# Optimization experiments

Hardware: AMD Instinct MI355X
Metric: run time of the kernel (lower is better)

## Reference

```python
import jax, jax.numpy as jnp
import numpy as np

D_MODEL = 128
D_STATE = 16
KCONV = 3
SQUEEZE = 16
NEIGH = 27
D_INNER = 2 * D_MODEL            # 256
C_CONV = D_INNER // SQUEEZE      # 16 conv3d output channels
D_SEQ = C_CONV * NEIGH           # 432 selective-scan channel dim
DT_RANK = int(np.ceil((D_MODEL // SQUEEZE * NEIGH) / 16))  # 14
LN_EPS = 1e-5


def setup_inputs() -> dict:
    key = jax.random.key(0)
    ks = jax.random.split(key, 10)
    B, Dd, H, W = 2, 16, 16, 16
    x = jax.random.normal(ks[0], (B, Dd, H, W, D_MODEL), dtype=jnp.float32)
    w_in = jax.random.normal(ks[1], (2 * D_INNER, D_MODEL), dtype=jnp.float32) * 0.02
    conv_w = jax.random.normal(ks[2], (C_CONV, SQUEEZE, KCONV, KCONV, KCONV), dtype=jnp.float32) * 0.05
    conv_b = jnp.zeros((C_CONV,), dtype=jnp.float32)
    x_proj_w = jax.random.normal(ks[3], (DT_RANK + 2 * D_STATE, D_SEQ), dtype=jnp.float32) * 0.05
    s = DT_RANK ** -0.5
    dt_w = jax.random.uniform(ks[4], (D_SEQ, DT_RANK), minval=-s, maxval=s, dtype=jnp.float32)
    # dt bias = inverse-softplus of dt ~ LogUniform[1e-3, 0.1]
    dt = jnp.exp(jax.random.uniform(ks[5], (D_SEQ,), dtype=jnp.float32)
                 * (np.log(0.1) - np.log(1e-3)) + np.log(1e-3))
    dt_b = dt + jnp.log(-jnp.expm1(-dt))
    A_logs = jnp.broadcast_to(jnp.log(jnp.arange(1, D_STATE + 1, dtype=jnp.float32)),
                              (D_SEQ, D_STATE)).copy()
    Ds = jnp.ones((D_SEQ,), dtype=jnp.float32)
    w_fold = jax.random.normal(ks[6], (D_INNER, D_SEQ), dtype=jnp.float32) * 0.05
    ln_g = jnp.ones((D_INNER,), dtype=jnp.float32)
    ln_b = jnp.zeros((D_INNER,), dtype=jnp.float32)
    w_out = jax.random.normal(ks[7], (D_MODEL, D_INNER), dtype=jnp.float32) * 0.05
    return dict(x=x, w_in=w_in, conv_w=conv_w, conv_b=conv_b, x_proj_w=x_proj_w,
                dt_w=dt_w, dt_b=dt_b, A_logs=A_logs, Ds=Ds, w_fold=w_fold,
                ln_g=ln_g, ln_b=ln_b, w_out=w_out)


def _selective_scan(u, delta, A, Bm, Cm, Dskip, delta_bias):
    # u, delta: (B, Dch, L); A: (Dch, N); Bm, Cm: (B, N, L); Dskip: (Dch,)
    delta = jax.nn.softplus(delta + delta_bias[None, :, None])
    a = jnp.exp(delta[..., None] * A[None, :, None, :])                     # (B,Dch,L,N)
    b = (delta * u)[..., None] * jnp.swapaxes(Bm, 1, 2)[:, None, :, :]      # (B,Dch,L,N)

    def combine(c1, c2):
        a1, b1 = c1
        a2, b2 = c2
        return a1 * a2, a2 * b1 + b2

    _, h = jax.lax.associative_scan(combine, (a, b), axis=2)                # (B,Dch,L,N)
    y = jnp.einsum('bdln,bnl->bdl', h, Cm)
    return y + Dskip[None, :, None] * u


def _unfold3(x):
    # x: (B, C, D, H, W) -> (B, C*27, D, H, W), channel-major, offset-minor
    B, C, Dd, H, W = x.shape
    p = KCONV // 2
    xp = jnp.pad(x, ((0, 0), (0, 0), (p, p), (p, p), (p, p)))
    taps = jnp.stack([xp[:, :, i:i + Dd, j:j + H, k:k + W]
                      for i in range(KCONV) for j in range(KCONV) for k in range(KCONV)],
                     axis=2)  # (B, C, 27, D, H, W)
    return taps.reshape(B, C * NEIGH, Dd, H, W)


def _forward(x, w_in, conv_w, conv_b, x_proj_w, dt_w, dt_b, A_logs, Ds,
             w_fold, ln_g, ln_b, w_out):
    B, Dd, H, W, _ = x.shape
    L = Dd * H * W
    xz = x @ w_in.T                                   # (B,D,H,W,512)
    xp, z = jnp.split(xz, 2, axis=-1)
    xc = jnp.transpose(xp, (0, 4, 1, 2, 3))           # (B,256,D,H,W)
    xc = jax.lax.conv_general_dilated(
        xc, conv_w, window_strides=(1, 1, 1), padding='SAME',
        dimension_numbers=('NCDHW', 'OIDHW', 'NCDHW'),
        feature_group_count=C_CONV) + conv_b[None, :, None, None, None]
    xc = jax.nn.silu(xc)                              # (B,16,D,H,W)
    xu = _unfold3(xc)                                 # (B,432,D,H,W)
    xs = xu.reshape(B, D_SEQ, L)
    x_dbl = jnp.einsum('bdl,cd->bcl', xs, x_proj_w)   # (B,46,L)
    dts = x_dbl[:, :DT_RANK]
    Bm = x_dbl[:, DT_RANK:DT_RANK + D_STATE]
    Cm = x_dbl[:, DT_RANK + D_STATE:]
    dts = jnp.einsum('brl,dr->bdl', dts, dt_w)        # (B,432,L)
    A = -jnp.exp(A_logs)
    y = _selective_scan(xs, dts, A, Bm, Cm, Ds, dt_b)  # (B,432,L)
    y = jnp.swapaxes(y, 1, 2).reshape(B, Dd, H, W, D_SEQ)
    y = y @ w_fold.T                                   # (B,D,H,W,256)
    mu = jnp.mean(y, axis=-1, keepdims=True)
    var = jnp.var(y, axis=-1, keepdims=True)
    y = (y - mu) * jax.lax.rsqrt(var + LN_EPS) * ln_g + ln_b
    y = y * jax.nn.silu(z)
    return y @ w_out.T                                 # (B,D,H,W,128)


def reference(x, w_in, conv_w, conv_b, x_proj_w, dt_w, dt_b, A_logs, Ds,
              w_fold, ln_g, ln_b, w_out):
    return _forward(x, w_in, conv_w, conv_b, x_proj_w, dt_w, dt_b, A_logs, Ds,
                    w_fold, ln_g, ln_b, w_out)
```

## Files before the change

kernel.cpp:

```cpp
#include <hip/hip_runtime.h>
#include <hip/hip_bf16.h>

#define DM     128
#define DSTATE 16
#define DINNER 256
#define CCONV  16
#define NEIGH  27
#define DSEQ   432
#define DTRANK 14
#define LVOL   4096
#define BATCH  2
#define NTOK   8192

typedef __attribute__((ext_vector_type(8))) unsigned short ushort8_t;
typedef __attribute__((ext_vector_type(8))) short short8_t;
typedef __attribute__((ext_vector_type(4))) float f32x4_t;

__device__ __forceinline__ float bf2f(unsigned short u) {
    union { unsigned int i; float f; } v; v.i = ((unsigned int)u) << 16; return v.f;
}
__device__ __forceinline__ unsigned short f2b(float f) {
    __hip_bfloat16 hb = __float2bfloat16(f);
    return *(unsigned short*)&hb;
}

__global__ void k_wprep(const float* __restrict__ w_in, const float* __restrict__ w_fold,
                        const float* __restrict__ w_out, float2* __restrict__ wint2,
                        unsigned short* __restrict__ wfb, unsigned short* __restrict__ wob) {
    int idx = blockIdx.x * 256 + threadIdx.x;
    if (idx < 32768) {
        int j = idx >> 8, t = idx & 255;
        wint2[idx] = make_float2(w_in[t * 128 + j], w_in[(t + 256) * 128 + j]);
    } else if (idx < 32768 + 114688) {
        int local = idx - 32768;
        int o = local / 448, dk = local - o * 448;
        wfb[local] = (dk < 432) ? f2b(w_fold[o * 432 + dk]) : (unsigned short)0;
    } else if (idx < 32768 + 114688 + 32768) {
        int local = idx - 32768 - 114688;
        wob[local] = f2b(w_out[local]);
    }
}

__global__ void k_inproj(const float* __restrict__ x, const float2* __restrict__ wint2,
                         float* __restrict__ xpt, float* __restrict__ zbuf) {
    int t = threadIdx.x;
    int tokbase = blockIdx.x * 16;
    int b = tokbase >> 12, lb = tokbase & 4095;
    __shared__ float xs_[16][128];
    for (int idx = t; idx < 2048; idx += 256)
        xs_[idx >> 7][idx & 127] = x[tokbase * 128 + idx];
    __syncthreads();
    float a0[16], a1[16];
#pragma unroll
    for (int k = 0; k < 16; k++) { a0[k] = 0.f; a1[k] = 0.f; }
    for (int j = 0; j < 128; j += 4) {
        float2 w0 = wint2[(j + 0) * 256 + t];
        float2 w1 = wint2[(j + 1) * 256 + t];
        float2 w2 = wint2[(j + 2) * 256 + t];
        float2 w3 = wint2[(j + 3) * 256 + t];
#pragma unroll
        for (int k = 0; k < 16; k++) {
            float4 xv = *(const float4*)&xs_[k][j];
            a0[k] += xv.x * w0.x + xv.y * w1.x + xv.z * w2.x + xv.w * w3.x;
            a1[k] += xv.x * w0.y + xv.y * w1.y + xv.z * w2.y + xv.w * w3.y;
        }
    }
    float* xr = xpt + (size_t)(b * 256 + t) * 4096 + lb;
#pragma unroll
    for (int k = 0; k < 16; k++) xr[k] = a0[k];
#pragma unroll
    for (int k = 0; k < 16; k++) zbuf[(tokbase + k) * 256 + t] = a1[k];
}

__global__ void k_conv(const float* __restrict__ xpt, const float* __restrict__ conv_w,
                       const float* __restrict__ conv_b, float* __restrict__ xc) {
    int t = threadIdx.x;
    int tok = blockIdx.x * 256 + t;
    int co = blockIdx.y;
    int b = tok >> 12, l = tok & 4095;
    int d0 = l >> 8, h0 = (l >> 4) & 15, w0 = l & 15;
    __shared__ float wl[432];
    for (int i = t; i < 432; i += 256) wl[i] = conv_w[co * 432 + i];
    __syncthreads();
    int nbo[27];
#pragma unroll
    for (int t27 = 0; t27 < 27; t27++) {
        int di = t27 / 9 - 1, dj = (t27 / 3) % 3 - 1, dk = t27 % 3 - 1;
        int zd = d0 + di, zh = h0 + dj, zw = w0 + dk;
        nbo[t27] = ((unsigned)zd > 15u || (unsigned)zh > 15u || (unsigned)zw > 15u)
                   ? -1 : ((zd << 8) + (zh << 4) + zw);
    }
    const float* xb = xpt + (size_t)(b * 256 + co * 16) * 4096;
    float acc0 = conv_b[co], acc1 = 0.f;
    for (int t27 = 0; t27 < 27; t27++) {
        int o = nbo[t27];
        if (o >= 0) {
#pragma unroll
            for (int q = 0; q < 16; q += 2) {
                acc0 += xb[q * 4096 + o]       * wl[q * 27 + t27];
                acc1 += xb[(q + 1) * 4096 + o] * wl[(q + 1) * 27 + t27];
            }
        }
    }
    float acc = acc0 + acc1;
    acc = acc / (1.f + __expf(-acc));
    xc[(b * 16 + co) * 4096 + l] = acc;
}

__global__ void k_xdbl(const float* __restrict__ xc, const float* __restrict__ x_proj_w,
                       float* __restrict__ dts, __hip_bfloat16* __restrict__ bc2) {
    int t = threadIdx.x;
    int tok = blockIdx.x * 256 + t;
    int c0 = blockIdx.y;
    int c1 = c0 + 23;
    int b = tok >> 12, l = tok & 4095;
    int d0 = l >> 8, h0 = (l >> 4) & 15, w0 = l & 15;
    __shared__ float wl0[432], wl1[432];
    for (int i = t; i < 432; i += 256) {
        wl0[i] = x_proj_w[c0 * 432 + i];
        wl1[i] = x_proj_w[c1 * 432 + i];
    }
    __syncthreads();
    int nbo[27];
#pragma unroll
    for (int t27 = 0; t27 < 27; t27++) {
        int di = t27 / 9 - 1, dj = (t27 / 3) % 3 - 1, dk = t27 % 3 - 1;
        int zd = d0 + di, zh = h0 + dj, zw = w0 + dk;
        nbo[t27] = ((unsigned)zd > 15u || (unsigned)zh > 15u || (unsigned)zw > 15u)
                   ? -1 : ((zd << 8) + (zh << 4) + zw);
    }
    const float* xcb = xc + b * 16 * 4096;
    float a00 = 0.f, a01 = 0.f, a10 = 0.f, a11 = 0.f;
    for (int t27 = 0; t27 < 27; t27++) {
        int o = nbo[t27];
        if (o >= 0) {
#pragma unroll
            for (int ch = 0; ch < 16; ch += 2) {
                float v0 = xcb[ch * 4096 + o];
                float v1 = xcb[(ch + 1) * 4096 + o];
                int i0 = ch * 27 + t27, i1 = (ch + 1) * 27 + t27;
                a00 += v0 * wl0[i0];
                a01 += v1 * wl0[i1];
                a10 += v0 * wl1[i0];
                a11 += v1 * wl1[i1];
            }
        }
    }
    float acc0 = a00 + a01;
    float acc1 = a10 + a11;
    if (c0 < 14)
        dts[(size_t)(b * 14 + c0) * 4096 + l] = acc0;
    else
        bc2[(size_t)(b * 32 + (c0 - 14)) * 4096 + l] = __float2bfloat16(acc0);
    bc2[(size_t)(b * 32 + (c1 - 14)) * 4096 + l] = __float2bfloat16(acc1);
}

__global__ __launch_bounds__(512, 2) void k_scan(
        const float* __restrict__ xc, const float* __restrict__ dts,
        const unsigned short* __restrict__ bc2, const float* __restrict__ dt_w,
        const float* __restrict__ dt_b, const float* __restrict__ A_logs,
        const float* __restrict__ Ds, unsigned short* __restrict__ y) {
    int bd = blockIdx.x;
    int b = bd / 432, dch = bd % 432;
    int t = threadIdx.x;
    int lane = t & 63, wv = t >> 6;

    bool intA = true;
#pragma unroll
    for (int n = 0; n < 16; n++) {
        float An = -__expf(A_logs[dch * 16 + n]);
        intA = intA && (fabsf(An + (float)(n + 1)) < 1e-3f);
    }
    float Dskip = Ds[dch];

    int cch = dch / 27, t27 = dch % 27;
    int di = t27 / 9 - 1, dj = (t27 / 3) % 3 - 1, dk = t27 % 3 - 1;

    float dtv[8];
    {
        float s[8];
        float bias = dt_b[dch];
#pragma unroll
        for (int i = 0; i < 8; i++) s[i] = bias;
        const float* dsb = dts + (size_t)(b * 14) * 4096 + t * 8;
#pragma unroll
        for (int r = 0; r < 14; r++) {
            float d8[8];
            *(float4*)&d8[0] = *(const float4*)(dsb + (size_t)r * 4096);
            *(float4*)&d8[4] = *(const float4*)(dsb + (size_t)r * 4096 + 4);
            float w = dt_w[dch * 14 + r];
#pragma unroll
            for (int i = 0; i < 8; i++) s[i] += d8[i] * w;
        }
#pragma unroll
        for (int i = 0; i < 8; i++)
            dtv[i] = (s[i] > 15.f) ? s[i] : log1pf(__expf(s[i]));
    }

    int d0 = t >> 5, h0 = (t >> 1) & 15, w0 = (t & 1) << 3;
    int zd = d0 + di, zh = h0 + dj;
    bool rowok = ((unsigned)zd <= 15u) && ((unsigned)zh <= 15u);
    const float* xr = xc + (size_t)(b * 16 + cch) * 4096 + (zd << 8) + (zh << 4);
    float dtu[8], ys[8];
#pragma unroll
    for (int i = 0; i < 8; i++) {
        int zw = w0 + i + dk;
        float u = (rowok && (unsigned)zw <= 15u) ? xr[zw] : 0.f;
        dtu[i] = dtv[i] * u;
        ys[i] = Dskip * u;
    }

    const unsigned short* bcb = bc2 + (size_t)(b * 32) * 4096 + t * 8;

    __shared__ float waggA[8][16], waggB[8][16];
    __shared__ float waggS[8];

    float h[16];
    float av[8];

    if (intA) {
        float aw[8];
#pragma unroll
        for (int i = 0; i < 8; i++) { av[i] = __expf(-dtv[i]); aw[i] = av[i]; }
        float sdt = ((dtv[0] + dtv[1]) + (dtv[2] + dtv[3]))
                  + ((dtv[4] + dtv[5]) + (dtv[6] + dtv[7]));

        float Bp[16];
        {
            ushort8_t Bnx = *(const ushort8_t*)(bcb);
#pragma unroll
            for (int n = 0; n < 16; n++) {
                ushort8_t Bv = Bnx;
                if (n < 15) Bnx = *(const ushort8_t*)(bcb + (size_t)(n + 1) * 4096);
                float bp = 0.f;
#pragma unroll
                for (int i = 0; i < 8; i++)
                    bp = aw[i] * bp + dtu[i] * bf2f(Bv[i]);
                Bp[n] = bp;
                if (n < 15) {
#pragma unroll
                    for (int i = 0; i < 8; i++) aw[i] *= av[i];
                }
            }
        }

#pragma unroll
        for (int s = 1; s < 64; s <<= 1) {
            float psdt = __shfl_up(sdt, s, 64);
            float pl = __expf(-sdt);
            float pb[16];
#pragma unroll
            for (int n = 0; n < 16; n++) pb[n] = __shfl_up(Bp[n], s, 64);
            if (lane >= s) {
                float pw = pl;
#pragma unroll
                for (int n = 0; n < 16; n++) {
                    Bp[n] = pw * pb[n] + Bp[n];
                    pw *= pl;
                }
                sdt += psdt;
            }
        }

        if (lane == 63) {
            waggS[wv] = sdt;
#pragma unroll
            for (int n = 0; n < 16; n++) waggB[wv][n] = Bp[n];
        }
        __syncthreads();

        float exsdt = __shfl_up(sdt, 1, 64);
        float exB[16];
#pragma unroll
        for (int n = 0; n < 16; n++) exB[n] = __shfl_up(Bp[n], 1, 64);
        if (lane == 0) {
            exsdt = 0.f;
#pragma unroll
            for (int n = 0; n < 16; n++) exB[n] = 0.f;
        }
        float WB[16];
#pragma unroll
        for (int n = 0; n < 16; n++) WB[n] = 0.f;
        for (int ww = 0; ww < wv; ww++) {
            float plw = __expf(-waggS[ww]);
            float pww = plw;
#pragma unroll
            for (int n = 0; n < 16; n++) {
                WB[n] = pww * WB[n] + waggB[ww][n];
                pww *= plw;
            }
        }
        float pex = __expf(-exsdt);
        float pwx = pex;
#pragma unroll
        for (int n = 0; n < 16; n++) {
            h[n] = pwx * WB[n] + exB[n];
            pwx *= pex;
        }
    } else {
        float A[16];
#pragma unroll
        for (int n = 0; n < 16; n++) A[n] = -__expf(A_logs[dch * 16 + n]);
        float Ap[16], Bp[16];
        ushort8_t Bnx = *(const ushort8_t*)(bcb);
#pragma unroll
        for (int n = 0; n < 16; n++) {
            ushort8_t Bv = Bnx;
            if (n < 15) Bnx = *(const ushort8_t*)(bcb + (size_t)(n + 1) * 4096);
            float ap = 1.f, bp = 0.f, An = A[n];
#pragma unroll
            for (int i = 0; i < 8; i++) {
                float a = __expf(dtv[i] * An);
                bp = a * bp + dtu[i] * bf2f(Bv[i]);
                ap *= a;
            }
            Ap[n] = ap; Bp[n] = bp;
        }
#pragma unroll
        for (int s = 1; s < 64; s <<= 1) {
#pragma unroll
            for (int n = 0; n < 16; n++) {
                float pa = __shfl_up(Ap[n], s, 64);
                float pb = __shfl_up(Bp[n], s, 64);
                if (lane >= s) {
                    Bp[n] = Ap[n] * pb + Bp[n];
                    Ap[n] *= pa;
                }
            }
        }
        if (lane == 63) {
#pragma unroll
            for (int n = 0; n < 16; n++) { waggA[wv][n] = Ap[n]; waggB[wv][n] = Bp[n]; }
        }
        __syncthreads();
#pragma unroll
        for (int n = 0; n < 16; n++) {
            float exA = __shfl_up(Ap[n], 1, 64);
            float exB = __shfl_up(Bp[n], 1, 64);
            if (lane == 0) { exA = 1.f; exB = 0.f; }
            float WB = 0.f;
            for (int ww = 0; ww < wv; ww++)
                WB = waggA[ww][n] * WB + waggB[ww][n];
            h[n] = exA * WB + exB;
        }
    }

    if (intA) {
        float aw[8];
#pragma unroll
        for (int i = 0; i < 8; i++) aw[i] = av[i];
        ushort8_t Bnx = *(const ushort8_t*)(bcb);
        ushort8_t Cnx = *(const ushort8_t*)(bcb + (size_t)16 * 4096);
#pragma unroll
        for (int n = 0; n < 16; n++) {
            ushort8_t Bv = Bnx, Cv = Cnx;
            if (n < 15) {
                Bnx = *(const ushort8_t*)(bcb + (size_t)(n + 1) * 4096);
                Cnx = *(const ushort8_t*)(bcb + (size_t)(17 + n) * 4096);
            }
            float hn = h[n];
#pragma unroll
            for (int i = 0; i < 8; i++) {
                hn = aw[i] * hn + dtu[i] * bf2f(Bv[i]);
                ys[i] += hn * bf2f(Cv[i]);
            }
            if (n < 15) {
#pragma unroll
                for (int i = 0; i < 8; i++) aw[i] *= av[i];
            }
        }
    } else {
        ushort8_t Bnx = *(const ushort8_t*)(bcb);
        ushort8_t Cnx = *(const ushort8_t*)(bcb + (size_t)16 * 4096);
#pragma unroll
        for (int n = 0; n < 16; n++) {
            float An = -__expf(A_logs[dch * 16 + n]);
            ushort8_t Bv = Bnx, Cv = Cnx;
            if (n < 15) {
                Bnx = *(const ushort8_t*)(bcb + (size_t)(n + 1) * 4096);
                Cnx = *(const ushort8_t*)(bcb + (size_t)(17 + n) * 4096);
            }
            float hn = h[n];
#pragma unroll
            for (int i = 0; i < 8; i++) {
                float a = __expf(dtv[i] * An);
                hn = a * hn + dtu[i] * bf2f(Bv[i]);
                ys[i] += hn * bf2f(Cv[i]);
            }
        }
    }

    unsigned short* yo = y + (size_t)(b * 432 + dch) * 4096 + t * 8;
    ushort8_t o8;
#pragma unroll
    for (int i = 0; i < 8; i++) o8[i] = f2b(ys[i]);
    *(ushort8_t*)yo = o8;
}

__global__ void k_tail(const unsigned short* __restrict__ y, const float* __restrict__ zbuf,
                       const unsigned short* __restrict__ wfb, const float* __restrict__ ln_g,
                       const float* __restrict__ ln_b, const unsigned short* __restrict__ wob,
                       float* __restrict__ out) {
    int t = threadIdx.x;
    int w = t >> 6;
    int l = t & 63;
    int lc = l & 15;
    int lr = l >> 4;
    int tokbase = blockIdx.x * 16;
    int b = tokbase >> 12, lbase = tokbase & 4095;

    __shared__ unsigned short Yt[16][456];
    __shared__ unsigned short Pt[16][264];
    __shared__ float red[4][16][2];

    for (int d = t; d < 448; d += 256) {
        if (d < 432) {
            const unsigned short* yr = y + (size_t)(b * 432 + d) * 4096 + lbase;
            ushort8_t v0 = *(const ushort8_t*)(yr);
            ushort8_t v1 = *(const ushort8_t*)(yr + 8);
#pragma unroll
            for (int j = 0; j < 8; j++) { Yt[j][d] = v0[j]; Yt[8 + j][d] = v1[j]; }
        } else {
#pragma unroll
            for (int j = 0; j < 16; j++) Yt[j][d] = 0;
        }
    }
    __syncthreads();

    f32x4_t acc[4];
#pragma unroll
    for (int m = 0; m < 4; m++) acc[m] = (f32x4_t){0.f, 0.f, 0.f, 0.f};
    for (int ks = 0; ks < 14; ks++) {
        int kb = ks * 32 + lr * 8;
        short8_t bf = *(const short8_t*)&Yt[lc][kb];
#pragma unroll
        for (int m = 0; m < 4; m++) {
            int outrow = (4 * w + m) * 16 + lc;
            short8_t af = *(const short8_t*)(wfb + (size_t)outrow * 448 + kb);
            acc[m] = __builtin_amdgcn_mfma_f32_16x16x32_bf16(af, bf, acc[m], 0, 0, 0);
        }
    }

    {
        float s = 0.f, s2 = 0.f;
#pragma unroll
        for (int m = 0; m < 4; m++) {
#pragma unroll
            for (int r = 0; r < 4; r++) { float v = acc[m][r]; s += v; s2 += v * v; }
        }
        s  += __shfl_xor(s, 16, 64);  s2 += __shfl_xor(s2, 16, 64);
        s  += __shfl_xor(s, 32, 64);  s2 += __shfl_xor(s2, 32, 64);
        if (l < 16) { red[w][l][0] = s; red[w][l][1] = s2; }
    }
    __syncthreads();
    float mu, rs;
    {
        float ts  = red[0][lc][0] + red[1][lc][0] + red[2][lc][0] + red[3][lc][0];
        float ts2 = red[0][lc][1] + red[1][lc][1] + red[2][lc][1] + red[3][lc][1];
        mu = ts * (1.f / 256.f);
        float var = ts2 * (1.f / 256.f) - mu * mu;
        rs = rsqrtf(var + 1e-5f);
    }

#pragma unroll
    for (int m = 0; m < 4; m++) {
#pragma unroll
        for (int r = 0; r < 4; r++) {
            int oidx = (4 * w + m) * 16 + lr * 4 + r;
            float g = ln_g[oidx], be = ln_b[oidx];
            float zv = zbuf[(tokbase + lc) * 256 + oidx];
            float sz = zv / (1.f + __expf(-zv));
            float p = ((acc[m][r] - mu) * rs * g + be) * sz;
            Pt[lc][oidx] = f2b(p);
        }
    }
    __syncthreads();

    f32x4_t oacc[2];
    oacc[0] = (f32x4_t){0.f, 0.f, 0.f, 0.f};
    oacc[1] = (f32x4_t){0.f, 0.f, 0.f, 0.f};
    for (int ks = 0; ks < 8; ks++) {
        int kb = ks * 32 + lr * 8;
        short8_t bf = *(const short8_t*)&Pt[lc][kb];
#pragma unroll
        for (int m = 0; m < 2; m++) {
            int orow = (2 * w + m) * 16 + lc;
            short8_t af = *(const short8_t*)(wob + (size_t)orow * 256 + kb);
            oacc[m] = __builtin_amdgcn_mfma_f32_16x16x32_bf16(af, bf, oacc[m], 0, 0, 0);
        }
    }
#pragma unroll
    for (int m = 0; m < 2; m++) {
        float o4[4];
#pragma unroll
        for (int r = 0; r < 4; r++) o4[r] = oacc[m][r];
        *(float4*)&out[(size_t)(tokbase + lc) * 128 + (2 * w + m) * 16 + lr * 4] = *(float4*)o4;
    }
}

extern "C" void kernel_launch(void* const* d_in, const int* in_sizes, int n_in,
                              void* d_out, int out_size, void* d_ws, size_t ws_size,
                              hipStream_t stream) {
    const float* x        = (const float*)d_in[0];
    const float* w_in     = (const float*)d_in[1];
    const float* conv_w   = (const float*)d_in[2];
    const float* conv_b   = (const float*)d_in[3];
    const float* x_proj_w = (const float*)d_in[4];
    const float* dt_w     = (const float*)d_in[5];
    const float* dt_b     = (const float*)d_in[6];
    const float* A_logs   = (const float*)d_in[7];
    const float* Ds       = (const float*)d_in[8];
    const float* w_fold   = (const float*)d_in[9];
    const float* ln_g     = (const float*)d_in[10];
    const float* ln_b     = (const float*)d_in[11];
    const float* w_out    = (const float*)d_in[12];
    float* out = (float*)d_out;

    float* ws     = (float*)d_ws;
    float* xpt    = ws;
    float* zbuf   = xpt    + 2097152;
    float* xc     = zbuf   + 2097152;
    float* dts    = xc     + 131072;
    float* bc2    = dts    + 114688;
    float* ybuf   = bc2    + 262144;
    float* wint   = ybuf   + 3538944;
    float* wfb    = wint   + 65536;
    float* wob    = wfb    + 57344;

    k_wprep<<<dim3(704), dim3(256), 0, stream>>>(w_in, w_fold, w_out, (float2*)wint,
                                                 (unsigned short*)wfb, (unsigned short*)wob);
    k_inproj<<<dim3(NTOK / 16), dim3(256), 0, stream>>>(x, (const float2*)wint, xpt, zbuf);
    k_conv<<<dim3(NTOK / 256, CCONV), dim3(256), 0, stream>>>(xpt, conv_w, conv_b, xc);
    k_xdbl<<<dim3(NTOK / 256, 23), dim3(256), 0, stream>>>(xc, x_proj_w, dts, (__hip_bfloat16*)bc2);
    k_scan<<<dim3(BATCH * DSEQ), dim3(512), 0, stream>>>(xc, dts, (const unsigned short*)bc2,
                                                         dt_w, dt_b, A_logs, Ds,
                                                         (unsigned short*)ybuf);
    k_tail<<<dim3(NTOK / 16), dim3(256), 0, stream>>>((const unsigned short*)ybuf, zbuf,
                                                      (const unsigned short*)wfb, ln_g, ln_b,
                                                      (const unsigned short*)wob, out);
}
```

Measured before the change: 147.9 us.

## Compute x_proj projection with bf16 MFMA over an LDS-staged unfolded tile

The x_dbl projection becomes a bf16 MFMA GEMM. Each block stages the 27-neighbour unfold of 32 tokens into LDS as bf16, and x_proj_w is pre-converted to a zero-padded bf16 buffer in the weight-prep kernel. This replaces the per-thread scalar fp32 dot products that re-gathered neighbours once for each of 23 channel pairs. The conv kernel also drops its LDS weight staging and reads weights straight from global memory. The cost is reduced precision on dts/B/C inputs, plus a serial gather loop in which only 176 threads do the second pass.

```diff
diff --git a/kernel.cpp b/kernel.cpp
--- a/kernel.cpp
+++ b/kernel.cpp
@@ -25,8 +25,9 @@
 }
 
 __global__ void k_wprep(const float* __restrict__ w_in, const float* __restrict__ w_fold,
-                        const float* __restrict__ w_out, float2* __restrict__ wint2,
-                        unsigned short* __restrict__ wfb, unsigned short* __restrict__ wob) {
+                        const float* __restrict__ w_out, const float* __restrict__ x_proj_w,
+                        float2* __restrict__ wint2, unsigned short* __restrict__ wfb,
+                        unsigned short* __restrict__ wob, unsigned short* __restrict__ wxpb) {
     int idx = blockIdx.x * 256 + threadIdx.x;
     if (idx < 32768) {
         int j = idx >> 8, t = idx & 255;
@@ -38,6 +39,10 @@
     } else if (idx < 32768 + 114688 + 32768) {
         int local = idx - 32768 - 114688;
         wob[local] = f2b(w_out[local]);
+    } else if (idx < 32768 + 114688 + 32768 + 21504) {
+        int local = idx - 32768 - 114688 - 32768;
+        int c = local / 448, dk = local - c * 448;
+        wxpb[local] = (c < 46 && dk < 432) ? f2b(x_proj_w[c * 432 + dk]) : (unsigned short)0;
     }
 }
 
@@ -79,9 +84,6 @@
     int co = blockIdx.y;
     int b = tok >> 12, l = tok & 4095;
     int d0 = l >> 8, h0 = (l >> 4) & 15, w0 = l & 15;
-    __shared__ float wl[432];
-    for (int i = t; i < 432; i += 256) wl[i] = conv_w[co * 432 + i];
-    __syncthreads();
     int nbo[27];
 #pragma unroll
     for (int t27 = 0; t27 < 27; t27++) {
@@ -91,14 +93,15 @@
                    ? -1 : ((zd << 8) + (zh << 4) + zw);
     }
     const float* xb = xpt + (size_t)(b * 256 + co * 16) * 4096;
+    const float* wr = conv_w + co * 432;
     float acc0 = conv_b[co], acc1 = 0.f;
     for (int t27 = 0; t27 < 27; t27++) {
         int o = nbo[t27];
         if (o >= 0) {
 #pragma unroll
             for (int q = 0; q < 16; q += 2) {
-                acc0 += xb[q * 4096 + o]       * wl[q * 27 + t27];
-                acc1 += xb[(q + 1) * 4096 + o] * wl[(q + 1) * 27 + t27];
+                acc0 += xb[q * 4096 + o]       * wr[q * 27 + t27];
+                acc1 += xb[(q + 1) * 4096 + o] * wr[(q + 1) * 27 + t27];
             }
         }
     }
@@ -107,52 +110,51 @@
     xc[(b * 16 + co) * 4096 + l] = acc;
 }
 
-__global__ void k_xdbl(const float* __restrict__ xc, const float* __restrict__ x_proj_w,
+__global__ void k_xdbl(const float* __restrict__ xc, const unsigned short* __restrict__ wxpb,
                        float* __restrict__ dts, __hip_bfloat16* __restrict__ bc2) {
     int t = threadIdx.x;
-    int tok = blockIdx.x * 256 + t;
-    int c0 = blockIdx.y;
-    int c1 = c0 + 23;
-    int b = tok >> 12, l = tok & 4095;
-    int d0 = l >> 8, h0 = (l >> 4) & 15, w0 = l & 15;
-    __shared__ float wl0[432], wl1[432];
-    for (int i = t; i < 432; i += 256) {
-        wl0[i] = x_proj_w[c0 * 432 + i];
-        wl1[i] = x_proj_w[c1 * 432 + i];
-    }
+    int w = t >> 6, l = t & 63;
+    int lc = l & 15, lr = l >> 4;
+    int tokbase = blockIdx.x * 32;
+    int b = tokbase >> 12, lbase = tokbase & 4095;
+
+    __shared__ unsigned short xsT[32][456];
+
+    for (int p = t; p < 432; p += 256) {
+        int ch = p / 27, tap = p - ch * 27;
+        int di = tap / 9 - 1, dj = (tap / 3) % 3 - 1, dk = tap % 3 - 1;
+        const float* xr = xc + (size_t)(b * 16 + ch) * 4096;
+        for (int tk = 0; tk < 32; tk++) {
+            int ll = lbase + tk;
+            int zd = (ll >> 8) + di, zh = ((ll >> 4) & 15) + dj, zw = (ll & 15) + dk;
+            float v = (((unsigned)zd <= 15u) && ((unsigned)zh <= 15u) && ((unsigned)zw <= 15u))
+                      ? xr[(zd << 8) + (zh << 4) + zw] : 0.f;
+            xsT[tk][p] = f2b(v);
+        }
+    }
+    for (int idx = t; idx < 16 * 32; idx += 256)
+        xsT[idx & 31][432 + (idx >> 5)] = 0;
     __syncthreads();
-    int nbo[27];
-#pragma unroll
-    for (int t27 = 0; t27 < 27; t27++) {
-        int di = t27 / 9 - 1, dj = (t27 / 3) % 3 - 1, dk = t27 % 3 - 1;
-        int zd = d0 + di, zh = h0 + dj, zw = w0 + dk;
-        nbo[t27] = ((unsigned)zd > 15u || (unsigned)zh > 15u || (unsigned)zw > 15u)
-                   ? -1 : ((zd << 8) + (zh << 4) + zw);
-    }
-    const float* xcb = xc + b * 16 * 4096;
-    float a00 = 0.f, a01 = 0.f, a10 = 0.f, a11 = 0.f;
-    for (int t27 = 0; t27 < 27; t27++) {
-        int o = nbo[t27];
-        if (o >= 0) {
-#pragma unroll
-            for (int ch = 0; ch < 16; ch += 2) {
-                float v0 = xcb[ch * 4096 + o];
-                float v1 = xcb[(ch + 1) * 4096 + o];
-                int i0 = ch * 27 + t27, i1 = (ch + 1) * 27 + t27;
-                a00 += v0 * wl0[i0];
-                a01 += v1 * wl0[i1];
-                a10 += v0 * wl1[i0];
-                a11 += v1 * wl1[i1];
-            }
-        }
-    }
-    float acc0 = a00 + a01;
-    float acc1 = a10 + a11;
-    if (c0 < 14)
-        dts[(size_t)(b * 14 + c0) * 4096 + l] = acc0;
-    else
-        bc2[(size_t)(b * 32 + (c0 - 14)) * 4096 + l] = __float2bfloat16(acc0);
-    bc2[(size_t)(b * 32 + (c1 - 14)) * 4096 + l] = __float2bfloat16(acc1);
+
+    for (int ti = w; ti < 6; ti += 4) {
+        int mt = ti % 3, nt = ti / 3;
+        f32x4_t acc = (f32x4_t){0.f, 0.f, 0.f, 0.f};
+        for (int ks = 0; ks < 14; ks++) {
+            int kb = ks * 32 + lr * 8;
+            short8_t bfr = *(const short8_t*)&xsT[nt * 16 + lc][kb];
+            short8_t afr = *(const short8_t*)(wxpb + (size_t)(mt * 16 + lc) * 448 + kb);
+            acc = __builtin_amdgcn_mfma_f32_16x16x32_bf16(afr, bfr, acc, 0, 0, 0);
+        }
+        int ltok = lbase + nt * 16 + lc;
+#pragma unroll
+        for (int r = 0; r < 4; r++) {
+            int c = mt * 16 + lr * 4 + r;
+            if (c < 14)
+                dts[(size_t)(b * 14 + c) * 4096 + ltok] = acc[r];
+            else if (c < 46)
+                bc2[(size_t)(b * 32 + (c - 14)) * 4096 + ltok] = __float2bfloat16(acc[r]);
+        }
+    }
 }
 
 __global__ __launch_bounds__(512, 2) void k_scan(
@@ -526,12 +528,15 @@
     float* wint   = ybuf   + 3538944;
     float* wfb    = wint   + 65536;
     float* wob    = wfb    + 57344;
-
-    k_wprep<<<dim3(704), dim3(256), 0, stream>>>(w_in, w_fold, w_out, (float2*)wint,
-                                                 (unsigned short*)wfb, (unsigned short*)wob);
+    float* wxpb   = wob    + 16384;
+
+    k_wprep<<<dim3(788), dim3(256), 0, stream>>>(w_in, w_fold, w_out, x_proj_w,
+                                                 (float2*)wint, (unsigned short*)wfb,
+                                                 (unsigned short*)wob, (unsigned short*)wxpb);
     k_inproj<<<dim3(NTOK / 16), dim3(256), 0, stream>>>(x, (const float2*)wint, xpt, zbuf);
     k_conv<<<dim3(NTOK / 256, CCONV), dim3(256), 0, stream>>>(xpt, conv_w, conv_b, xc);
-    k_xdbl<<<dim3(NTOK / 256, 23), dim3(256), 0, stream>>>(xc, x_proj_w, dts, (__hip_bfloat16*)bc2);
+    k_xdbl<<<dim3(NTOK / 32), dim3(256), 0, stream>>>(xc, (const unsigned short*)wxpb,
+                                                      dts, (__hip_bfloat16*)bc2);
     k_scan<<<dim3(BATCH * DSEQ), dim3(512), 0, stream>>>(xc, dts, (const unsigned short*)bc2,
                                                          dt_w, dt_b, A_logs, Ds,
                                                          (unsigned short*)ybuf);
```

After: 142.3 us. 3.8% less time.
